# Performance work log

Hardware: AMD Instinct MI355X
Metric: run time of the kernel (lower is better)

The kernel has to match this reference:

```python
import jax, jax.numpy as jnp
import numpy as np

B, D, E, H, T = 16384, 1024, 8, 512, 256
NUM_TASKS = 3  # purchase, quality, price


def setup_inputs() -> dict:
    key = jax.random.key(0)
    ks = jax.random.split(key, 12)
    s_in = 1.0 / np.sqrt(D)
    s_h = 1.0 / np.sqrt(H)
    s_t = 1.0 / np.sqrt(T)
    return {
        "x": jax.random.normal(ks[0], (B, D), dtype=jnp.float32),
        # expert layer 1: [E, D, H], layer 2: [E, H, H]
        "We1": jax.random.uniform(ks[1], (E, D, H), jnp.float32, -s_in, s_in),
        "be1": jax.random.uniform(ks[2], (E, H), jnp.float32, -s_in, s_in),
        "We2": jax.random.uniform(ks[3], (E, H, H), jnp.float32, -s_h, s_h),
        "be2": jax.random.uniform(ks[4], (E, H), jnp.float32, -s_h, s_h),
        # gates (one per task): [T_tasks, D, E]
        "Wg": jax.random.uniform(ks[5], (NUM_TASKS, D, E), jnp.float32, -s_in, s_in),
        "bg": jax.random.uniform(ks[6], (NUM_TASKS, E), jnp.float32, -s_in, s_in),
        # towers: [T_tasks, H, T] then [T_tasks, T, 1]
        "Wt1": jax.random.uniform(ks[7], (NUM_TASKS, H, T), jnp.float32, -s_h, s_h),
        "bt1": jax.random.uniform(ks[8], (NUM_TASKS, T), jnp.float32, -s_h, s_h),
        "Wt2": jax.random.uniform(ks[9], (NUM_TASKS, T, 1), jnp.float32, -s_t, s_t),
        "bt2": jax.random.uniform(ks[10], (NUM_TASKS, 1), jnp.float32, -s_t, s_t),
    }


def reference(x, We1, be1, We2, be2, Wg, bg, Wt1, bt1, Wt2, bt2):
    # Batched expert MLPs (dropout = identity in eval): [B, E, H]
    h1 = jax.nn.relu(jnp.einsum("bd,edh->beh", x, We1) + be1)
    expert_out = jax.nn.relu(jnp.einsum("beh,ehk->bek", h1, We2) + be2)
    # Per-task softmax gates: [T, B, E]
    gates = jax.nn.softmax(jnp.einsum("bd,tde->tbe", x, Wg) + bg[:, None, :], axis=-1)
    # Weighted combine: [T, B, H]
    task_in = jnp.einsum("tbe,beh->tbh", gates, expert_out)
    # Towers: [T, B, 1]
    th = jax.nn.relu(jnp.einsum("tbh,thk->tbk", task_in, Wt1) + bt1[:, None, :])
    preds = jax.nn.sigmoid(jnp.einsum("tbk,tko->tbo", th, Wt2) + bt2[:, None, :])
    return (preds[0], preds[1], preds[2])
```

## Files before the change

### kernel.cpp

```cpp
#include <hip/hip_runtime.h>


#define BM 128
#define BN 128
#define BK 64

typedef __attribute__((ext_vector_type(8))) short short8;
typedef __attribute__((ext_vector_type(4))) float floatx4;
typedef __attribute__((ext_vector_type(4))) unsigned short ushortx4;
typedef __attribute__((ext_vector_type(8))) unsigned short ushortx8;

__device__ __forceinline__ unsigned short f32_to_bf16(float f) {
  unsigned int u = __float_as_uint(f);
  u += 0x7fffu + ((u >> 16) & 1u);
  return (unsigned short)(u >> 16);
}
__device__ __forceinline__ float bf16_to_f32(unsigned short h) {
  return __uint_as_float(((unsigned int)h) << 16);
}

__device__ __forceinline__ void async_cp16(const void* g, void* lds) {
  __builtin_amdgcn_global_load_lds(
      (const __attribute__((address_space(1))) void*)g,
      (__attribute__((address_space(3))) void*)lds, 16, 0, 0);
}

__global__ void cvt_x_kernel(const float* __restrict__ x, unsigned short* __restrict__ xb) {
  size_t i = ((size_t)blockIdx.x * blockDim.x + threadIdx.x) * 4;
  floatx4 v = *(const floatx4*)(x + i);
  ushortx4 o;
#pragma unroll
  for (int j = 0; j < 4; j++) o[j] = f32_to_bf16(v[j]);
  *(ushortx4*)(xb + i) = o;
}

__global__ void transpose_cvt_kernel(const float* __restrict__ in,
                                     unsigned short* __restrict__ out,
                                     int K, int N) {
  __shared__ float tile[32][33];
  const size_t zoff = (size_t)blockIdx.z * K * N;
  int n0 = blockIdx.x * 32, k0 = blockIdx.y * 32;
  for (int i = threadIdx.y; i < 32; i += 8)
    tile[i][threadIdx.x] = in[zoff + (size_t)(k0 + i) * N + n0 + threadIdx.x];
  __syncthreads();
  for (int i = threadIdx.y; i < 32; i += 8)
    out[zoff + (size_t)(n0 + i) * K + k0 + threadIdx.x] = f32_to_bf16(tile[threadIdx.x][i]);
}

__global__ void transpose_wg_kernel(const float* __restrict__ in, float* __restrict__ out) {
  int idx = blockIdx.x * 256 + threadIdx.x;
  int t = idx >> 13, r = idx & 8191;
  int e = r >> 10, d = r & 1023;
  out[idx] = in[t * 8192 + d * 8 + e];
}

__global__ __launch_bounds__(256) void gates_kernel(
    const float* __restrict__ x, const float* __restrict__ WgT,
    const float* __restrict__ bg, float* __restrict__ gout) {
  int wave = threadIdx.x >> 6, lane = threadIdx.x & 63;
  int b = blockIdx.x * 4 + wave;
  const float* xr = x + (size_t)b * 1024;
  float xv[16];
#pragma unroll
  for (int j = 0; j < 16; j++) xv[j] = xr[lane + 64 * j];
  float mylogit = 0.f;
#pragma unroll
  for (int te = 0; te < 24; te++) {
    const float* w = WgT + te * 1024;
    float a = 0.f;
#pragma unroll
    for (int j = 0; j < 16; j++) a += xv[j] * w[lane + 64 * j];
#pragma unroll
    for (int off = 32; off > 0; off >>= 1) a += __shfl_xor(a, off, 64);
    if (lane == te) mylogit = a;
  }
  if (lane < 24) {
    int t = lane >> 3, e = lane & 7;
    float logit = mylogit + bg[lane];
    float m = logit;
    m = fmaxf(m, __shfl_xor(m, 4, 64));
    m = fmaxf(m, __shfl_xor(m, 2, 64));
    m = fmaxf(m, __shfl_xor(m, 1, 64));
    float ex = __expf(logit - m);
    float s = ex;
    s += __shfl_xor(s, 4, 64);
    s += __shfl_xor(s, 2, 64);
    s += __shfl_xor(s, 1, 64);
    gout[(size_t)t * 131072 + (size_t)b * 8 + e] = ex / s;
  }
}

__global__ __launch_bounds__(256) void gemm_bt_relu(
    const unsigned short* __restrict__ Abase, long aOffZ, int lda,
    const unsigned short* __restrict__ Bbase, long bOffZ,
    const float* __restrict__ biasBase, int biasOffZ,
    unsigned short* __restrict__ Cbase, long cOffZ, int ldc,
    int K) {
  __shared__ __align__(16) unsigned short As[BM * BK];
  __shared__ __align__(16) unsigned short Bs[BN * BK];
  const int tid = threadIdx.x;
  const int z = blockIdx.z;
  const unsigned short* A = Abase + (size_t)aOffZ * z + (size_t)blockIdx.x * BM * lda;
  const unsigned short* Bt = Bbase + (size_t)bOffZ * z + (size_t)blockIdx.y * BN * K;
  const float* bias = biasBase + (size_t)biasOffZ * z + blockIdx.y * BN;
  unsigned short* C = Cbase + (size_t)cOffZ * z + (size_t)blockIdx.x * BM * ldc + blockIdx.y * BN;

  const int wave = tid >> 6, lane = tid & 63;
  const int wm = (wave >> 1) * 64, wn = (wave & 1) * 64;
  const int lm = lane & 15, lq = lane >> 4;
  const int sw = lm & 7;

  floatx4 acc[4][4] = {};

  const int sr = tid >> 3;
  const int sc = (((tid & 7) ^ (sr & 7)) << 3);

  for (int kt = 0; kt < K; kt += BK) {
#pragma unroll
    for (int i = 0; i < 4; i++)
      async_cp16(A + (size_t)(sr + 32 * i) * lda + kt + sc,
                 (char*)As + i * 4096 + tid * 16);
#pragma unroll
    for (int i = 0; i < 4; i++)
      async_cp16(Bt + (size_t)(sr + 32 * i) * K + kt + sc,
                 (char*)Bs + i * 4096 + tid * 16);
    __syncthreads();
#pragma unroll
    for (int ks = 0; ks < 2; ks++) {
      short8 af[4], bf[4];
      const int ch = ((ks * 4 + lq) ^ sw) << 3;
#pragma unroll
      for (int i = 0; i < 4; i++)
        af[i] = *(const short8*)(As + (wm + 16 * i + lm) * BK + ch);
#pragma unroll
      for (int j = 0; j < 4; j++)
        bf[j] = *(const short8*)(Bs + (wn + 16 * j + lm) * BK + ch);
#pragma unroll
      for (int i = 0; i < 4; i++)
#pragma unroll
        for (int j = 0; j < 4; j++)
          acc[i][j] = __builtin_amdgcn_mfma_f32_16x16x32_bf16(af[i], bf[j], acc[i][j], 0, 0, 0);
    }
    __syncthreads();
  }

#pragma unroll
  for (int i = 0; i < 4; i++) {
    const int row = wm + 16 * i + lq * 4;
#pragma unroll
    for (int j = 0; j < 4; j++) {
      const int col = wn + 16 * j + lm;
      const float bv = bias[col];
#pragma unroll
      for (int v = 0; v < 4; v++) {
        float val = fmaxf(acc[i][j][v] + bv, 0.0f);
        C[(size_t)(row + v) * ldc + col] = f32_to_bf16(val);
      }
    }
  }
}

__global__ void combine_kernel(const unsigned short* __restrict__ eo,
                               const float* __restrict__ gates,
                               unsigned short* __restrict__ ti,
                               int b0, int Bc) {
  int tid = blockIdx.x * 256 + threadIdx.x;
  int bl = tid >> 6;
  int hc = (tid & 63) << 3;
  float g[3][8];
#pragma unroll
  for (int t = 0; t < 3; t++) {
    const floatx4* gp = (const floatx4*)(gates + ((size_t)t * 16384 + b0 + bl) * 8);
    floatx4 g0 = gp[0], g1 = gp[1];
#pragma unroll
    for (int j = 0; j < 4; j++) { g[t][j] = g0[j]; g[t][4 + j] = g1[j]; }
  }
  float out[3][8] = {};
#pragma unroll
  for (int e = 0; e < 8; e++) {
    ushortx8 v = *(const ushortx8*)(eo + ((size_t)bl * 8 + e) * 512 + hc);
#pragma unroll
    for (int j = 0; j < 8; j++) {
      float f = bf16_to_f32(v[j]);
#pragma unroll
      for (int t = 0; t < 3; t++) out[t][j] += g[t][e] * f;
    }
  }
#pragma unroll
  for (int t = 0; t < 3; t++) {
    ushortx8 o;
#pragma unroll
    for (int j = 0; j < 8; j++) o[j] = f32_to_bf16(out[t][j]);
    *(ushortx8*)(ti + ((size_t)t * Bc + bl) * 512 + hc) = o;
  }
}

__global__ void tower2_kernel(const unsigned short* __restrict__ th,
                              const float* __restrict__ Wt2,
                              const float* __restrict__ bt2,
                              float* __restrict__ out,
                              int b0, int bcShift) {
  int wave = threadIdx.x >> 6, lane = threadIdx.x & 63;
  int row = blockIdx.x * 4 + wave;
  int t = row >> bcShift;
  int bl = row & ((1 << bcShift) - 1);
  const unsigned short* r = th + (size_t)row * 256;
  int k = lane * 4;
  ushortx4 v = *(const ushortx4*)(r + k);
  float a = 0.f;
#pragma unroll
  for (int j = 0; j < 4; j++) a += bf16_to_f32(v[j]) * Wt2[t * 256 + k + j];
#pragma unroll
  for (int off = 32; off > 0; off >>= 1) a += __shfl_xor(a, off, 64);
  if (lane == 0) out[(t << 14) + b0 + bl] = 1.f / (1.f + __expf(-(a + bt2[t])));
}

extern "C" void kernel_launch(void* const* d_in, const int* in_sizes, int n_in,
                              void* d_out, int out_size, void* d_ws, size_t ws_size,
                              hipStream_t stream) {
  (void)in_sizes; (void)n_in; (void)out_size;
  const float* x   = (const float*)d_in[0];
  const float* We1 = (const float*)d_in[1];
  const float* be1 = (const float*)d_in[2];
  const float* We2 = (const float*)d_in[3];
  const float* be2 = (const float*)d_in[4];
  const float* Wg  = (const float*)d_in[5];
  const float* bg  = (const float*)d_in[6];
  const float* Wt1 = (const float*)d_in[7];
  const float* bt1 = (const float*)d_in[8];
  const float* Wt2 = (const float*)d_in[9];
  const float* bt2 = (const float*)d_in[10];
  float* out = (float*)d_out;

  char* ws = (char*)d_ws;
  unsigned short* xb   = (unsigned short*)(ws + 0);
  unsigned short* W1T  = (unsigned short*)(ws + 33554432);
  unsigned short* W2T  = (unsigned short*)(ws + 41943040);
  unsigned short* Wt1T = (unsigned short*)(ws + 46137344);
  float*          gts  = (float*)(ws + 46923776);
  float*          WgT  = (float*)(ws + 48496640);
  const size_t fixed = 48594944;

  size_t rem = ws_size > fixed ? ws_size - fixed : 0;
  int Bc = 8192;
  while (Bc > 512 && (size_t)Bc * 20992 > rem) Bc >>= 1;
  const int nc = 16384 / Bc;
  int bcShift = 0;
  while ((1 << bcShift) < Bc) bcShift++;

  char* cb = ws + fixed;
  unsigned short* h1c = (unsigned short*)(cb);
  unsigned short* eoc = (unsigned short*)(cb + (size_t)Bc * 8192);
  unsigned short* tic = (unsigned short*)(cb + (size_t)Bc * 16384);
  unsigned short* thc = (unsigned short*)(cb + (size_t)Bc * 16384 + (size_t)Bc * 3072);

  cvt_x_kernel<<<16384, 256, 0, stream>>>(x, xb);
  transpose_cvt_kernel<<<dim3(16, 32, 8), dim3(32, 8), 0, stream>>>(We1, W1T, 1024, 512);
  transpose_cvt_kernel<<<dim3(16, 16, 8), dim3(32, 8), 0, stream>>>(We2, W2T, 512, 512);
  transpose_cvt_kernel<<<dim3(8, 16, 3),  dim3(32, 8), 0, stream>>>(Wt1, Wt1T, 512, 256);
  transpose_wg_kernel<<<96, 256, 0, stream>>>(Wg, WgT);
  gates_kernel<<<4096, 256, 0, stream>>>(x, WgT, bg, gts);

  for (int c = 0; c < nc; c++) {
    const unsigned short* xbc = xb + (size_t)c * Bc * 1024;
    gemm_bt_relu<<<dim3(Bc / 128, 4, 8), 256, 0, stream>>>(
        xbc, 0L, 1024, W1T, 524288L, be1, 512, h1c, 512L, 4096, 1024);
    gemm_bt_relu<<<dim3(Bc / 128, 4, 8), 256, 0, stream>>>(
        h1c, 512L, 4096, W2T, 262144L, be2, 512, eoc, 512L, 4096, 512);
    combine_kernel<<<Bc / 4, 256, 0, stream>>>(eoc, gts, tic, c * Bc, Bc);
    gemm_bt_relu<<<dim3(Bc / 128, 2, 3), 256, 0, stream>>>(
        tic, (long)Bc * 512, 512, Wt1T, 131072L, bt1, 256, thc, (long)Bc * 256, 256, 512);
    tower2_kernel<<<3 * Bc / 4, 256, 0, stream>>>(thc, Wt2, bt2, out, c * Bc, bcShift);
  }
}
```

Before: 521.4 us.

## Fuse tower GEMM with tower2, merge prep kernels, fold x conversion into gates

Replaces the tower-1 GEMM plus separate tower2 dot-product kernel with one MFMA kernel. It applies bias, ReLU and the Wt2 dot product in the epilogue, reduces across waves through LDS and writes the sigmoid output directly, so the th intermediate buffer is never written. The four weight transpose/convert launches become a single prep kernel, and the bf16 conversion of x is folded into the gates kernel. Dropping the th buffer lowers per-row workspace, so the chunk size can grow to cover the whole batch and fewer loop iterations and launches are needed. The fused tower kernel has no double buffering, and the 128-row tile gives only 384 blocks.

```diff
diff --git a/kernel.cpp b/kernel.cpp
--- a/kernel.cpp
+++ b/kernel.cpp
@@ -25,44 +25,53 @@
       (__attribute__((address_space(3))) void*)lds, 16, 0, 0);
 }
 
-__global__ void cvt_x_kernel(const float* __restrict__ x, unsigned short* __restrict__ xb) {
-  size_t i = ((size_t)blockIdx.x * blockDim.x + threadIdx.x) * 4;
-  floatx4 v = *(const floatx4*)(x + i);
-  ushortx4 o;
-#pragma unroll
-  for (int j = 0; j < 4; j++) o[j] = f32_to_bf16(v[j]);
-  *(ushortx4*)(xb + i) = o;
-}
-
-__global__ void transpose_cvt_kernel(const float* __restrict__ in,
-                                     unsigned short* __restrict__ out,
-                                     int K, int N) {
-  __shared__ float tile[32][33];
-  const size_t zoff = (size_t)blockIdx.z * K * N;
+__device__ __forceinline__ void transpose_slice(
+    const float* __restrict__ in, unsigned short* __restrict__ out,
+    int K, int N, float (*tile)[33]) {
   int n0 = blockIdx.x * 32, k0 = blockIdx.y * 32;
   for (int i = threadIdx.y; i < 32; i += 8)
-    tile[i][threadIdx.x] = in[zoff + (size_t)(k0 + i) * N + n0 + threadIdx.x];
+    tile[i][threadIdx.x] = in[(size_t)(k0 + i) * N + n0 + threadIdx.x];
   __syncthreads();
   for (int i = threadIdx.y; i < 32; i += 8)
-    out[zoff + (size_t)(n0 + i) * K + k0 + threadIdx.x] = f32_to_bf16(tile[threadIdx.x][i]);
-}
-
-__global__ void transpose_wg_kernel(const float* __restrict__ in, float* __restrict__ out) {
-  int idx = blockIdx.x * 256 + threadIdx.x;
-  int t = idx >> 13, r = idx & 8191;
-  int e = r >> 10, d = r & 1023;
-  out[idx] = in[t * 8192 + d * 8 + e];
-}
-
-__global__ __launch_bounds__(256) void gates_kernel(
+    out[(size_t)(n0 + i) * K + k0 + threadIdx.x] = f32_to_bf16(tile[threadIdx.x][i]);
+}
+
+__global__ void prep_kernel(const float* __restrict__ We1, const float* __restrict__ We2,
+                            const float* __restrict__ Wt1, const float* __restrict__ Wg,
+                            unsigned short* __restrict__ W1T, unsigned short* __restrict__ W2T,
+                            unsigned short* __restrict__ Wt1T, float* __restrict__ WgT) {
+  __shared__ float tile[32][33];
+  int z = blockIdx.z;
+  if (z < 8) {
+    transpose_slice(We1 + (size_t)z * 524288, W1T + (size_t)z * 524288, 1024, 512, tile);
+  } else if (z < 16) {
+    if (blockIdx.y < 16)
+      transpose_slice(We2 + (size_t)(z - 8) * 262144, W2T + (size_t)(z - 8) * 262144, 512, 512, tile);
+  } else if (z < 19) {
+    if (blockIdx.x < 8 && blockIdx.y < 16)
+      transpose_slice(Wt1 + (size_t)(z - 16) * 131072, Wt1T + (size_t)(z - 16) * 131072, 512, 256, tile);
+  } else {
+    if (blockIdx.x < 16 && blockIdx.y < 6) {
+      int idx = (blockIdx.y * 16 + blockIdx.x) * 256 + threadIdx.y * 32 + threadIdx.x;
+      int t = idx >> 13, r = idx & 8191, e = r >> 10, d = r & 1023;
+      WgT[idx] = Wg[t * 8192 + d * 8 + e];
+    }
+  }
+}
+
+__global__ __launch_bounds__(256) void gates_cvt_kernel(
     const float* __restrict__ x, const float* __restrict__ WgT,
-    const float* __restrict__ bg, float* __restrict__ gout) {
+    const float* __restrict__ bg, float* __restrict__ gout,
+    unsigned short* __restrict__ xb) {
   int wave = threadIdx.x >> 6, lane = threadIdx.x & 63;
   int b = blockIdx.x * 4 + wave;
   const float* xr = x + (size_t)b * 1024;
   float xv[16];
 #pragma unroll
   for (int j = 0; j < 16; j++) xv[j] = xr[lane + 64 * j];
+  unsigned short* xbr = xb + (size_t)b * 1024;
+#pragma unroll
+  for (int j = 0; j < 16; j++) xbr[lane + 64 * j] = f32_to_bf16(xv[j]);
   float mylogit = 0.f;
 #pragma unroll
   for (int te = 0; te < 24; te++) {
@@ -195,24 +204,87 @@
   }
 }
 
-__global__ void tower2_kernel(const unsigned short* __restrict__ th,
-                              const float* __restrict__ Wt2,
-                              const float* __restrict__ bt2,
-                              float* __restrict__ out,
-                              int b0, int bcShift) {
-  int wave = threadIdx.x >> 6, lane = threadIdx.x & 63;
-  int row = blockIdx.x * 4 + wave;
-  int t = row >> bcShift;
-  int bl = row & ((1 << bcShift) - 1);
-  const unsigned short* r = th + (size_t)row * 256;
-  int k = lane * 4;
-  ushortx4 v = *(const ushortx4*)(r + k);
-  float a = 0.f;
-#pragma unroll
-  for (int j = 0; j < 4; j++) a += bf16_to_f32(v[j]) * Wt2[t * 256 + k + j];
-#pragma unroll
-  for (int off = 32; off > 0; off >>= 1) a += __shfl_xor(a, off, 64);
-  if (lane == 0) out[(t << 14) + b0 + bl] = 1.f / (1.f + __expf(-(a + bt2[t])));
+__global__ __launch_bounds__(512) void tower_fused_kernel(
+    const unsigned short* __restrict__ tic, const unsigned short* __restrict__ Wt1T,
+    const float* __restrict__ bt1, const float* __restrict__ Wt2,
+    const float* __restrict__ bt2, float* __restrict__ out,
+    int b0, int Bc) {
+  __shared__ __align__(16) unsigned short As[128 * 64];
+  __shared__ __align__(16) unsigned short Bs[256 * 64];
+  const int tid = threadIdx.x;
+  const int mtiles = Bc >> 7;
+  const int t = blockIdx.x / mtiles;
+  const int xbl = blockIdx.x % mtiles;
+  const unsigned short* A = tic + ((size_t)t * Bc + (size_t)xbl * 128) * 512;
+  const unsigned short* Bt = Wt1T + (size_t)t * 131072;
+
+  const int wave = tid >> 6, lane = tid & 63;
+  const int wm = (wave >> 2) * 64, wn = (wave & 3) * 64;
+  const int lm = lane & 15, lq = lane >> 4;
+  const int sw = lm & 7;
+
+  floatx4 acc[4][4] = {};
+
+  const int sr = tid >> 3;
+  const int sc = (((tid & 7) ^ (sr & 7)) << 3);
+
+  for (int kt = 0; kt < 512; kt += 64) {
+#pragma unroll
+    for (int i = 0; i < 2; i++)
+      async_cp16(A + (size_t)(sr + 64 * i) * 512 + kt + sc,
+                 (char*)As + i * 8192 + tid * 16);
+#pragma unroll
+    for (int i = 0; i < 4; i++)
+      async_cp16(Bt + (size_t)(sr + 64 * i) * 512 + kt + sc,
+                 (char*)Bs + i * 8192 + tid * 16);
+    __syncthreads();
+#pragma unroll
+    for (int ks = 0; ks < 2; ks++) {
+      short8 af[4], bf[4];
+      const int ch = ((ks * 4 + lq) ^ sw) << 3;
+#pragma unroll
+      for (int i = 0; i < 4; i++)
+        af[i] = *(const short8*)(As + (wm + 16 * i + lm) * 64 + ch);
+#pragma unroll
+      for (int j = 0; j < 4; j++)
+        bf[j] = *(const short8*)(Bs + (wn + 16 * j + lm) * 64 + ch);
+#pragma unroll
+      for (int i = 0; i < 4; i++)
+#pragma unroll
+        for (int j = 0; j < 4; j++)
+          acc[i][j] = __builtin_amdgcn_mfma_f32_16x16x32_bf16(af[i], bf[j], acc[i][j], 0, 0, 0);
+    }
+    __syncthreads();
+  }
+
+  float b1v[4], w2v[4];
+#pragma unroll
+  for (int j = 0; j < 4; j++) {
+    int col = wn + 16 * j + lm;
+    b1v[j] = bt1[t * 256 + col];
+    w2v[j] = Wt2[t * 256 + col];
+  }
+  float* pt = (float*)As;
+#pragma unroll
+  for (int i = 0; i < 4; i++) {
+#pragma unroll
+    for (int v = 0; v < 4; v++) {
+      float p = 0.f;
+#pragma unroll
+      for (int j = 0; j < 4; j++)
+        p += fmaxf(acc[i][j][v] + b1v[j], 0.0f) * w2v[j];
+      p += __shfl_xor(p, 1, 64);
+      p += __shfl_xor(p, 2, 64);
+      p += __shfl_xor(p, 4, 64);
+      p += __shfl_xor(p, 8, 64);
+      if (lm == 0) pt[(wm + 16 * i + lq * 4 + v) * 4 + (wave & 3)] = p;
+    }
+  }
+  __syncthreads();
+  if (tid < 128) {
+    float s = pt[tid * 4] + pt[tid * 4 + 1] + pt[tid * 4 + 2] + pt[tid * 4 + 3] + bt2[t];
+    out[(t << 14) + b0 + xbl * 128 + tid] = 1.f / (1.f + __expf(-s));
+  }
 }
 
 extern "C" void kernel_launch(void* const* d_in, const int* in_sizes, int n_in,
@@ -242,24 +314,17 @@
   const size_t fixed = 48594944;
 
   size_t rem = ws_size > fixed ? ws_size - fixed : 0;
-  int Bc = 8192;
-  while (Bc > 512 && (size_t)Bc * 20992 > rem) Bc >>= 1;
+  int Bc = 16384;
+  while (Bc > 512 && (size_t)Bc * 19456 > rem) Bc >>= 1;
   const int nc = 16384 / Bc;
-  int bcShift = 0;
-  while ((1 << bcShift) < Bc) bcShift++;
 
   char* cb = ws + fixed;
   unsigned short* h1c = (unsigned short*)(cb);
   unsigned short* eoc = (unsigned short*)(cb + (size_t)Bc * 8192);
   unsigned short* tic = (unsigned short*)(cb + (size_t)Bc * 16384);
-  unsigned short* thc = (unsigned short*)(cb + (size_t)Bc * 16384 + (size_t)Bc * 3072);
-
-  cvt_x_kernel<<<16384, 256, 0, stream>>>(x, xb);
-  transpose_cvt_kernel<<<dim3(16, 32, 8), dim3(32, 8), 0, stream>>>(We1, W1T, 1024, 512);
-  transpose_cvt_kernel<<<dim3(16, 16, 8), dim3(32, 8), 0, stream>>>(We2, W2T, 512, 512);
-  transpose_cvt_kernel<<<dim3(8, 16, 3),  dim3(32, 8), 0, stream>>>(Wt1, Wt1T, 512, 256);
-  transpose_wg_kernel<<<96, 256, 0, stream>>>(Wg, WgT);
-  gates_kernel<<<4096, 256, 0, stream>>>(x, WgT, bg, gts);
+
+  prep_kernel<<<dim3(16, 32, 20), dim3(32, 8), 0, stream>>>(We1, We2, Wt1, Wg, W1T, W2T, Wt1T, WgT);
+  gates_cvt_kernel<<<4096, 256, 0, stream>>>(x, WgT, bg, gts, xb);
 
   for (int c = 0; c < nc; c++) {
     const unsigned short* xbc = xb + (size_t)c * Bc * 1024;
@@ -268,8 +333,7 @@
     gemm_bt_relu<<<dim3(Bc / 128, 4, 8), 256, 0, stream>>>(
         h1c, 512L, 4096, W2T, 262144L, be2, 512, eoc, 512L, 4096, 512);
     combine_kernel<<<Bc / 4, 256, 0, stream>>>(eoc, gts, tic, c * Bc, Bc);
-    gemm_bt_relu<<<dim3(Bc / 128, 2, 3), 256, 0, stream>>>(
-        tic, (long)Bc * 512, 512, Wt1T, 131072L, bt1, 256, thc, (long)Bc * 256, 256, 512);
-    tower2_kernel<<<3 * Bc / 4, 256, 0, stream>>>(thc, Wt2, bt2, out, c * Bc, bcShift);
-  }
-}
+    tower_fused_kernel<<<3 * (Bc / 128), 512, 0, stream>>>(
+        tic, Wt1T, bt1, Wt2, bt2, out, c * Bc, Bc);
+  }
+}
```

New measurement: 498.1 us. 4.5% less time.
